# Kernel tuning notes

Measured on AMD Instinct MI355X. Metric: run time of the kernel, lower is better.

The kernel has to match this reference:

```python
import jax, jax.numpy as jnp
import numpy as np

N_NODES = 100000

def gcn_conv(x, W, b, src, dst):
    # PyG GCNConv: h = x @ W; add self-loops; symmetric norm D^-1/2 A D^-1/2; scatter-add; + bias
    n = x.shape[0]
    h = x @ W  # transform first (out_dim small) -> cheap messages
    loop = jnp.arange(n, dtype=src.dtype)
    s = jnp.concatenate([src, loop])
    d = jnp.concatenate([dst, loop])
    deg = jax.ops.segment_sum(jnp.ones_like(d, dtype=h.dtype), d, num_segments=n)
    dinv = jnp.where(deg > 0, jax.lax.rsqrt(deg), 0.0)
    norm = dinv[s] * dinv[d]  # [E+N]
    msg = h[s] * norm[:, None]  # gather + scale
    out = jax.ops.segment_sum(msg, d, num_segments=n)  # scatter-add to targets
    return out + b

def setup_inputs() -> dict:
    key = jax.random.key(0)
    k1, k2, k3, k4 = jax.random.split(key, 4)
    x = jax.random.normal(k1, (N_NODES, 128), dtype=jnp.float32)
    edge_index = jax.random.randint(k2, (2, 3200000), 0, N_NODES, dtype=jnp.int64)
    W1 = jax.random.normal(k3, (128, 16), dtype=jnp.float32) * 0.1
    b1 = jnp.zeros((16,), dtype=jnp.float32)
    W2 = jax.random.normal(k4, (16, 7), dtype=jnp.float32) * 0.1
    b2 = jnp.zeros((7,), dtype=jnp.float32)
    return {"x": x, "edge_index": edge_index, "W1": W1, "b1": b1, "W2": W2, "b2": b2}

def reference(x, edge_index, W1, b1, W2, b2):
    src, dst = edge_index[0], edge_index[1]
    h = gcn_conv(x, W1, b1, src, dst)
    h = jax.nn.relu(h)
    # F.dropout(training=self.training) is identity in eval mode
    h = gcn_conv(h, W2, b2, src, dst)
    return jax.nn.log_softmax(h, axis=1)
```

## Files before the change

kernel.cpp:

```cpp
#include <hip/hip_runtime.h>
#include <hip/hip_bf16.h>
#include <hip/hip_fp16.h>
#include <math.h>


#define FIN 128
#define FMID 16
#define FOUT 7

#define LBITS 7
#define NPB   128
#define SBITS 17
#define SMASK 0x1FFFF
#define NB_MAX 800
#define CAP   5120
#define EPT   12
#define BINT  1024
#define TILE  (EPT * BINT)

#define G1N   128
#define AS1   17
#define AS2   9

__global__ void zero_kernel(int* __restrict__ p, int m) {
    int i = blockIdx.x * 256 + threadIdx.x;
    if (i < m) p[i] = 0;
}

__device__ inline void addh8(float* a, float4 v) {
    const __half2* h = (const __half2*)&v;
#pragma unroll
    for (int k = 0; k < 4; ++k) {
        float2 f = __half22float2(h[k]);
        a[2 * k]     += f.x;
        a[2 * k + 1] += f.y;
    }
}

__global__ __launch_bounds__(BINT) void bin_kernel(const int* __restrict__ src,
                                                   const int* __restrict__ dst,
                                                   int* __restrict__ pairs,
                                                   int* __restrict__ gcnt,
                                                   int e, int nb) {
    __shared__ int sorted[TILE];
    __shared__ int cnt[NB_MAX], excl[NB_MAX], lofs[NB_MAX], gbase[NB_MAX];
    __shared__ int wsum[16];
    int tid = threadIdx.x;
    for (int j = tid; j < nb; j += BINT) cnt[j] = 0;
    __syncthreads();

    int base = blockIdx.x * TILE;
    int w[EPT], bk[EPT];
#pragma unroll
    for (int k = 0; k < EPT; ++k) {
        int idx = base + k * BINT + tid;
        if (idx < e) {
            int d = dst[idx], s = src[idx];
            w[k]  = ((d & (NPB - 1)) << SBITS) | s;
            bk[k] = d >> LBITS;
            atomicAdd(&cnt[bk[k]], 1);
        } else bk[k] = -1;
    }
    __syncthreads();

    if (tid < nb && cnt[tid] > 0) gbase[tid] = atomicAdd(&gcnt[tid], cnt[tid]);

    {
        int v = (tid < nb) ? cnt[tid] : 0;
        int lane = tid & 63, wid = tid >> 6;
        int incl = v;
#pragma unroll
        for (int d = 1; d < 64; d <<= 1) {
            int t = __shfl_up(incl, d);
            if (lane >= d) incl += t;
        }
        if (lane == 63) wsum[wid] = incl;
        __syncthreads();
        if (tid < 16) {
            int wv = wsum[tid];
            int wincl = wv;
#pragma unroll
            for (int d = 1; d < 16; d <<= 1) {
                int t = __shfl_up(wincl, d);
                if (tid >= d) wincl += t;
            }
            wsum[tid] = wincl - wv;
        }
        __syncthreads();
        if (tid < nb) {
            int ex = wsum[wid] + incl - v;
            excl[tid] = ex;
            lofs[tid] = ex;
        }
    }
    __syncthreads();

#pragma unroll
    for (int k = 0; k < EPT; ++k) {
        if (bk[k] >= 0) {
            int pos = atomicAdd(&lofs[bk[k]], 1);
            sorted[pos] = w[k];
        }
    }
    __syncthreads();

    int g16 = tid >> 4, l16 = tid & 15;
    for (int j = g16; j < nb; j += 64) {
        int c = cnt[j];
        if (!c) continue;
        int st = excl[j], gb = gbase[j];
        size_t go = (size_t)j * CAP;
        for (int l = l16; l < c; l += 16)
            if (gb + l < CAP) pairs[go + gb + l] = sorted[st + l];
    }
}

__global__ __launch_bounds__(512) void sort_kernel(int* __restrict__ pairs,
                                                   const int* __restrict__ gcnt,
                                                   int* __restrict__ rs_g,
                                                   float* __restrict__ dinv, int n) {
    __shared__ int slist[CAP];
    __shared__ int cnt2[NPB * 2], lofs2[NPB * 2], rowstart[NPB];
    __shared__ int wtot_s;
    int tid = threadIdx.x, b = blockIdx.x;
    int cc = tid & 1;
    if (tid < NPB * 2) cnt2[tid] = 0;
    __syncthreads();

    int c = min(gcnt[b], CAP);
    size_t go = (size_t)b * CAP;

    for (int i = tid; i < c; i += 512)
        atomicAdd(&cnt2[(pairs[go + i] >> SBITS) * 2 + cc], 1);
    __syncthreads();

    int v = 0, incl = 0;
    if (tid < NPB) {
        v = cnt2[tid * 2] + cnt2[tid * 2 + 1];
        incl = v;
        int lane = tid & 63;
#pragma unroll
        for (int d = 1; d < 64; d <<= 1) {
            int t = __shfl_up(incl, d);
            if (lane >= d) incl += t;
        }
        if (tid == 63) wtot_s = incl;
    }
    __syncthreads();
    if (tid < NPB) {
        int ex = incl - v + ((tid >= 64) ? wtot_s : 0);
        rowstart[tid] = ex;
        lofs2[tid * 2]     = ex;
        lofs2[tid * 2 + 1] = ex + cnt2[tid * 2];
    }
    __syncthreads();

    for (int i = tid; i < c; i += 512) {
        int w = pairs[go + i];
        int pos = atomicAdd(&lofs2[(w >> SBITS) * 2 + cc], 1);
        slist[pos] = w & SMASK;
    }
    __syncthreads();

    for (int i = tid; i < c; i += 512) pairs[go + i] = slist[i];
    if (tid < NPB) {
        rs_g[b * NPB + tid] = rowstart[tid];
        int node = b * NPB + tid;
        if (node < n) dinv[node] = rsqrtf((float)v + 1.0f);
    }
}

__global__ __launch_bounds__(256) void gemm1_kernel(const float* __restrict__ x,
                                                    const float* __restrict__ W,
                                                    const float* __restrict__ dinv,
                                                    __half* __restrict__ h1h, int n,
                                                    int sentinel) {
    __shared__ float WsT[16 * 132];
    int tid = threadIdx.x;
    int n0 = blockIdx.x * G1N;

    for (int i = tid; i < FIN * FMID; i += 256) {
        int k = i >> 4, f = i & 15;
        WsT[f * 132 + k] = W[i];
    }
    __syncthreads();

    int ngrp = tid >> 3;
    int fh = tid & 7;
    int r0 = n0 + ngrp, r1 = r0 + 32, r2 = r0 + 64, r3 = r0 + 96;
    int nc = n - 1;
    size_t c0 = (size_t)min(r0, nc) * 32;
    size_t c1 = (size_t)min(r1, nc) * 32;
    size_t c2 = (size_t)min(r2, nc) * 32;
    size_t c3 = (size_t)min(r3, nc) * 32;

    const float4* x4  = (const float4*)x;
    const float4* wa4 = (const float4*)(WsT + (2 * fh) * 132);
    const float4* wb4 = (const float4*)(WsT + (2 * fh + 1) * 132);

    float a0 = 0.f, a1 = 0.f, a2 = 0.f, a3 = 0.f;
    float b0 = 0.f, b1_ = 0.f, b2_ = 0.f, b3 = 0.f;

#pragma unroll 8
    for (int ck = 0; ck < 32; ++ck) {
        float4 x0 = x4[c0 + ck];
        float4 x1 = x4[c1 + ck];
        float4 x2 = x4[c2 + ck];
        float4 x3 = x4[c3 + ck];
        float4 wa = wa4[ck];
        float4 wb = wb4[ck];
        a0 += x0.x * wa.x + x0.y * wa.y + x0.z * wa.z + x0.w * wa.w;
        a1 += x1.x * wa.x + x1.y * wa.y + x1.z * wa.z + x1.w * wa.w;
        a2 += x2.x * wa.x + x2.y * wa.y + x2.z * wa.z + x2.w * wa.w;
        a3 += x3.x * wa.x + x3.y * wa.y + x3.z * wa.z + x3.w * wa.w;
        b0  += x0.x * wb.x + x0.y * wb.y + x0.z * wb.z + x0.w * wb.w;
        b1_ += x1.x * wb.x + x1.y * wb.y + x1.z * wb.z + x1.w * wb.w;
        b2_ += x2.x * wb.x + x2.y * wb.y + x2.z * wb.z + x2.w * wb.w;
        b3  += x3.x * wb.x + x3.y * wb.y + x3.z * wb.z + x3.w * wb.w;
    }

    float ra[4] = {a0, a1, a2, a3};
    float rb[4] = {b0, b1_, b2_, b3};
    int rr[4] = {r0, r1, r2, r3};
    __half2* h2 = (__half2*)h1h;
#pragma unroll
    for (int i = 0; i < 4; ++i) {
        int node = rr[i];
        if (node < n) {
            float dd = dinv ? dinv[node] : 1.0f;
            h2[(size_t)node * 8 + fh] = __floats2half2_rn(ra[i] * dd, rb[i] * dd);
        } else if (node == n && sentinel) {
            h2[(size_t)n * 8 + fh] = __floats2half2_rn(0.0f, 0.0f);
        }
    }
}

__global__ __launch_bounds__(512) void scatter1_kernel(const int* __restrict__ pairs,
                                                       const int* __restrict__ gcnt,
                                                       const int* __restrict__ rs_g,
                                                       const float* __restrict__ dinv,
                                                       const __half* __restrict__ h1h,
                                                       const float* __restrict__ b1,
                                                       const float* __restrict__ W2,
                                                       __half* __restrict__ h3h, int n) {
    __shared__ int   slist[CAP + 8];
    __shared__ int   rowstart_s[NPB + 1];
    __shared__ float acc2[NPB * AS1];
    __shared__ float W2s[FMID * FOUT];
    __shared__ float b1s[FMID];
    int tid = threadIdx.x, b = blockIdx.x;
    int c = min(gcnt[b], CAP);
    size_t go = (size_t)b * CAP;

    if (tid < FMID * FOUT) W2s[tid] = W2[tid];
    if (tid < FMID) b1s[tid] = b1[tid];
    if (tid < NPB) rowstart_s[tid] = rs_g[b * NPB + tid];
    if (tid == 0) rowstart_s[NPB] = c;
    for (int i = tid; i < c; i += 512) slist[i] = pairs[go + i];
    __syncthreads();

    {
        int nd = tid >> 2, l = tid & 3;
        int eo = l >> 1, half = l & 1;
        int pbeg = rowstart_s[nd];
        int pend = rowstart_s[nd + 1];
        const float4* h4 = (const float4*)h1h;
        float acc[8];
#pragma unroll
        for (int k = 0; k < 8; ++k) acc[k] = 0.0f;
        for (int p = pbeg + eo; p < pend; p += 8) {
            int i0 = slist[p];
            int i1 = (p + 2 < pend) ? slist[p + 2] : n;
            int i2 = (p + 4 < pend) ? slist[p + 4] : n;
            int i3 = (p + 6 < pend) ? slist[p + 6] : n;
            float4 v0 = h4[(size_t)i0 * 2 + half];
            float4 v1 = h4[(size_t)i1 * 2 + half];
            float4 v2 = h4[(size_t)i2 * 2 + half];
            float4 v3 = h4[(size_t)i3 * 2 + half];
            addh8(acc, v0);
            addh8(acc, v1);
            addh8(acc, v2);
            addh8(acc, v3);
        }
#pragma unroll
        for (int k = 0; k < 8; ++k) acc[k] += __shfl_xor(acc[k], 2);
        if (eo == 0) {
            float* ap = acc2 + nd * AS1 + half * 8;
#pragma unroll
            for (int k = 0; k < 8; ++k) ap[k] = acc[k];
        }
    }
    __syncthreads();

    int node = b * NPB + tid;
    if (tid < NPB && node < n) {
        float dd = dinv[node];
        float4 sr0 = ((const float4*)h1h)[(size_t)node * 2 + 0];
        float4 sr1 = ((const float4*)h1h)[(size_t)node * 2 + 1];
        float fself[FMID];
        {
            const __half2* ha = (const __half2*)&sr0;
            const __half2* hb = (const __half2*)&sr1;
#pragma unroll
            for (int k = 0; k < 4; ++k) {
                float2 fa = __half22float2(ha[k]);
                float2 fb = __half22float2(hb[k]);
                fself[2 * k]     = fa.x;
                fself[2 * k + 1] = fa.y;
                fself[8 + 2 * k]     = fb.x;
                fself[8 + 2 * k + 1] = fb.y;
            }
        }
        float vbuf[FMID];
#pragma unroll
        for (int k = 0; k < FMID; ++k) {
            float t = dd * (acc2[tid * AS1 + k] + fself[k]) + b1s[k];
            vbuf[k] = t > 0.0f ? t : 0.0f;
        }
        float sj[8];
#pragma unroll
        for (int j = 0; j < FOUT; ++j) {
            float s = 0.0f;
#pragma unroll
            for (int k = 0; k < FMID; ++k) s += vbuf[k] * W2s[k * FOUT + j];
            sj[j] = s * dd;
        }
        float4 st;
        __half2* sp = (__half2*)&st;
        sp[0] = __floats2half2_rn(sj[0], sj[1]);
        sp[1] = __floats2half2_rn(sj[2], sj[3]);
        sp[2] = __floats2half2_rn(sj[4], sj[5]);
        sp[3] = __floats2half2_rn(sj[6], 0.0f);
        ((float4*)h3h)[node] = st;
    } else if (tid < NPB && node == n) {
        ((float4*)h3h)[n] = make_float4(0.f, 0.f, 0.f, 0.f);
    }
}

__global__ __launch_bounds__(512) void scatter2_kernel(const int* __restrict__ pairs,
                                                       const int* __restrict__ gcnt,
                                                       const int* __restrict__ rs_g,
                                                       const float* __restrict__ dinv,
                                                       const __half* __restrict__ h3h,
                                                       const float* __restrict__ b2,
                                                       float* __restrict__ out, int n) {
    __shared__ int   slist[CAP + 8];
    __shared__ int   rowstart_s[NPB + 1];
    __shared__ float acc2[NPB * AS2];
    __shared__ float b2s[8];
    int tid = threadIdx.x, b = blockIdx.x;
    int c = min(gcnt[b], CAP);
    size_t go = (size_t)b * CAP;

    if (tid < FOUT) b2s[tid] = b2[tid];
    if (tid < NPB) rowstart_s[tid] = rs_g[b * NPB + tid];
    if (tid == 0) rowstart_s[NPB] = c;
    for (int i = tid; i < c; i += 512) slist[i] = pairs[go + i];
    __syncthreads();

    {
        int nd = tid >> 2, l = tid & 3;
        int pbeg = rowstart_s[nd];
        int pend = rowstart_s[nd + 1];
        const float4* h4 = (const float4*)h3h;
        float acc[8];
#pragma unroll
        for (int k = 0; k < 8; ++k) acc[k] = 0.0f;
        for (int p = pbeg + l; p < pend; p += 8) {
            int i0 = slist[p];
            int i1 = (p + 4 < pend) ? slist[p + 4] : n;
            float4 v0 = h4[i0];
            float4 v1 = h4[i1];
            addh8(acc, v0);
            addh8(acc, v1);
        }
#pragma unroll
        for (int k = 0; k < 8; ++k) {
            acc[k] += __shfl_xor(acc[k], 1);
            acc[k] += __shfl_xor(acc[k], 2);
        }
        if (l == 0) {
            float* ap = acc2 + nd * AS2;
#pragma unroll
            for (int k = 0; k < 8; ++k) ap[k] = acc[k];
        }
    }
    __syncthreads();

    int node = b * NPB + tid;
    if (tid < NPB && node < n) {
        float dd = dinv[node];
        float4 sv = ((const float4*)h3h)[node];
        float hself[8];
        {
            const __half2* h = (const __half2*)&sv;
#pragma unroll
            for (int k = 0; k < 4; ++k) {
                float2 f2v = __half22float2(h[k]);
                hself[2 * k] = f2v.x;
                hself[2 * k + 1] = f2v.y;
            }
        }
        float t[FOUT], m = -INFINITY;
#pragma unroll
        for (int j = 0; j < FOUT; ++j) {
            t[j] = dd * (acc2[tid * AS2 + j] + hself[j]) + b2s[j];
            m = fmaxf(m, t[j]);
        }
        float sum = 0.0f;
#pragma unroll
        for (int j = 0; j < FOUT; ++j) sum += expf(t[j] - m);
        float lse = logf(sum);
#pragma unroll
        for (int j = 0; j < FOUT; ++j) out[(size_t)node * FOUT + j] = t[j] - m - lse;
    }
}

__global__ void fb_gemm1_kernel(const float* __restrict__ x, const float* __restrict__ W,
                                float* __restrict__ h1, int n) {
    int i = blockIdx.x * blockDim.x + threadIdx.x;
    if (i >= n * FMID) return;
    int node = i >> 4, f = i & 15;
    float s = 0.0f;
    for (int k = 0; k < FIN; ++k) s += x[(size_t)node * FIN + k] * W[k * FMID + f];
    h1[i] = s;
}
__global__ void fb_deg_kernel(const int* __restrict__ dst, float* __restrict__ deg, int e) {
    int i = blockIdx.x * blockDim.x + threadIdx.x;
    if (i < e) atomicAdd(&deg[dst[i]], 1.0f);
}
__global__ void fb_dinv_kernel(float* __restrict__ deg, int n) {
    int i = blockIdx.x * blockDim.x + threadIdx.x;
    if (i < n) deg[i] = rsqrtf(deg[i] + 1.0f);
}
__global__ void fb_scatter1_kernel(const int* __restrict__ src, const int* __restrict__ dst,
                                   const float* __restrict__ dinv, const float* __restrict__ h1,
                                   float* __restrict__ out1, int e) {
    int i = blockIdx.x * blockDim.x + threadIdx.x;
    if (i >= e) return;
    int s = src[i], d = dst[i];
    float norm = dinv[s] * dinv[d];
    const float4* hs = (const float4*)(h1 + (size_t)s * FMID);
    float* o = out1 + (size_t)d * FMID;
#pragma unroll
    for (int q = 0; q < 4; ++q) {
        float4 vv = hs[q];
        atomicAdd(o + q * 4 + 0, vv.x * norm);
        atomicAdd(o + q * 4 + 1, vv.y * norm);
        atomicAdd(o + q * 4 + 2, vv.z * norm);
        atomicAdd(o + q * 4 + 3, vv.w * norm);
    }
}
__global__ void fb_layer2_kernel(const float* __restrict__ agg, const float* __restrict__ h1,
                                 const float* __restrict__ dinv, const float* __restrict__ b1,
                                 const float* __restrict__ W2, float* __restrict__ h3, int n) {
    int i = blockIdx.x * blockDim.x + threadIdx.x;
    if (i >= n) return;
    float dii = dinv[i] * dinv[i];
    float v[FMID];
#pragma unroll
    for (int k = 0; k < FMID; ++k) {
        float t = agg[(size_t)i * FMID + k] + h1[(size_t)i * FMID + k] * dii + b1[k];
        v[k] = t > 0.0f ? t : 0.0f;
    }
#pragma unroll
    for (int j = 0; j < FOUT; ++j) {
        float s = 0.0f;
#pragma unroll
        for (int k = 0; k < FMID; ++k) s += v[k] * W2[k * FOUT + j];
        h3[(size_t)i * FOUT + j] = s;
    }
}
__global__ void fb_scatter2_kernel(const int* __restrict__ src, const int* __restrict__ dst,
                                   const float* __restrict__ dinv, const float* __restrict__ h3,
                                   float* __restrict__ out2, int e) {
    int i = blockIdx.x * blockDim.x + threadIdx.x;
    if (i >= e) return;
    int s = src[i], d = dst[i];
    float norm = dinv[s] * dinv[d];
    const float* hs = h3 + (size_t)s * FOUT;
    float* o = out2 + (size_t)d * FOUT;
#pragma unroll
    for (int j = 0; j < FOUT; ++j) atomicAdd(o + j, hs[j] * norm);
}
__global__ void fb_finalize_kernel(const float* __restrict__ agg2, const float* __restrict__ h3,
                                   const float* __restrict__ dinv, const float* __restrict__ b2,
                                   float* __restrict__ out, int n) {
    int i = blockIdx.x * blockDim.x + threadIdx.x;
    if (i >= n) return;
    float dii = dinv[i] * dinv[i];
    float t[FOUT], m = -INFINITY;
#pragma unroll
    for (int j = 0; j < FOUT; ++j) {
        t[j] = agg2[(size_t)i * FOUT + j] + h3[(size_t)i * FOUT + j] * dii + b2[j];
        m = fmaxf(m, t[j]);
    }
    float sum = 0.0f;
#pragma unroll
    for (int j = 0; j < FOUT; ++j) sum += expf(t[j] - m);
    float lse = logf(sum);
#pragma unroll
    for (int j = 0; j < FOUT; ++j) out[(size_t)i * FOUT + j] = t[j] - m - lse;
}

extern "C" void kernel_launch(void* const* d_in, const int* in_sizes, int n_in,
                              void* d_out, int out_size, void* d_ws, size_t ws_size,
                              hipStream_t stream) {
    const float* x  = (const float*)d_in[0];
    const int*   ei = (const int*)d_in[1];
    const float* W1 = (const float*)d_in[2];
    const float* b1 = (const float*)d_in[3];
    const float* W2 = (const float*)d_in[4];
    const float* b2 = (const float*)d_in[5];

    const int n = in_sizes[0] / FIN;
    const int e = in_sizes[1] / 2;
    const int* src = ei;
    const int* dst = ei + e;

    const int nb  = (n + NPB - 1) / NPB;
    const int nb2 = (n + 1 + NPB - 1) / NPB;

    size_t need = ((size_t)NB_MAX + (size_t)nb * CAP + (size_t)n +
                   (size_t)nb2 * NPB + (size_t)8 * (n + 1) + (size_t)4 * (n + 1)) * 4;

    if (nb2 <= NB_MAX && n + 1 < (1 << SBITS) && ws_size >= need) {
        int*    gcnt  = (int*)d_ws;
        int*    pairs = gcnt + NB_MAX;
        float*  dinv  = (float*)(pairs + (size_t)nb * CAP);
        int*    rs_g  = (int*)(dinv + n);
        __half* h1h   = (__half*)(rs_g + (size_t)nb2 * NPB);
        __half* h3h   = h1h + (size_t)16 * (n + 1);

        zero_kernel<<<(NB_MAX + 255) / 256, 256, 0, stream>>>(gcnt, NB_MAX);

        int gridBin = (e + TILE - 1) / TILE;
        bin_kernel<<<gridBin, BINT, 0, stream>>>(src, dst, pairs, gcnt, e, nb);
        sort_kernel<<<nb, 512, 0, stream>>>(pairs, gcnt, rs_g, dinv, n);
        gemm1_kernel<<<nb2, 256, 0, stream>>>(x, W1, dinv, h1h, n, 1);
        scatter1_kernel<<<nb2, 512, 0, stream>>>(pairs, gcnt, rs_g, dinv, h1h, b1, W2, h3h, n);
        scatter2_kernel<<<nb, 512, 0, stream>>>(pairs, gcnt, rs_g, dinv, h3h, b2, (float*)d_out, n);
    } else {
        float* ws   = (float*)d_ws;
        float* deg  = ws;
        float* out1 = ws + (size_t)n;
        float* out2 = ws + (size_t)17 * n;
        float* h1   = ws + (size_t)24 * n;
        float* h3   = ws + (size_t)40 * n;

        hipMemsetAsync(ws, 0, (size_t)24 * n * sizeof(float), stream);

        const int B = 256;
        const int gridE = (e + B - 1) / B;
        const int gridN = (n + B - 1) / B;
        fb_deg_kernel<<<gridE, B, 0, stream>>>(dst, deg, e);
        fb_dinv_kernel<<<gridN, B, 0, stream>>>(deg, n);
        fb_gemm1_kernel<<<(n * FMID + B - 1) / B, B, 0, stream>>>(x, W1, h1, n);
        fb_scatter1_kernel<<<gridE, B, 0, stream>>>(src, dst, deg, h1, out1, e);
        fb_layer2_kernel<<<gridN, B, 0, stream>>>(out1, h1, deg, b1, W2, h3, n);
        fb_scatter2_kernel<<<gridE, B, 0, stream>>>(src, dst, deg, h3, out2, e);
        fb_finalize_kernel<<<gridN, B, 0, stream>>>(out2, h3, deg, b2, (float*)d_out, n);
    }
}
```

Measured before the change: 104.5 us.

## Fuse GCN pipeline into one cooperative persistent kernel with grid syncs

Replaces the six separate launches (zero, bin, sort, gemm1, scatter1, scatter2) with a single cooperative mega-kernel of 768 persistent blocks that separates the phases with grid-wide syncs. The aim is to remove kernel launch gaps and tail effects between phases. The binning phase now uses a smaller per-block tile with 512 threads. It also adds host-side occupancy and attribute queries on every call, and grid.sync has its own cost. It falls back to the old path if the cooperative launch is not possible.

New measurement: 104.7 us. About the same (+0.3%).

```diff
diff --git a/kernel.cpp b/kernel.cpp
--- a/kernel.cpp
+++ b/kernel.cpp
@@ -1,7 +1,10 @@
 #include <hip/hip_runtime.h>
 #include <hip/hip_bf16.h>
 #include <hip/hip_fp16.h>
+#include <hip/hip_cooperative_groups.h>
 #include <math.h>
+
+namespace cg = cooperative_groups;
 
 
 #define FIN 128
@@ -14,20 +17,20 @@
 #define SMASK 0x1FFFF
 #define NB_MAX 800
 #define CAP   5120
+#define AS1   17
+#define AS2   9
+
+#define MGRID 768
+#define MBLK  512
+#define BIN_TILE 5120
+#define SMEM_BYTES ((BIN_TILE + 4 * NB_MAX + 16) * 4)
+
 #define EPT   12
 #define BINT  1024
 #define TILE  (EPT * BINT)
-
 #define G1N   128
-#define AS1   17
-#define AS2   9
-
-__global__ void zero_kernel(int* __restrict__ p, int m) {
-    int i = blockIdx.x * 256 + threadIdx.x;
-    if (i < m) p[i] = 0;
-}
-
-__device__ inline void addh8(float* a, float4 v) {
+
+__device__ __forceinline__ void addh8(float* a, float4 v) {
     const __half2* h = (const __half2*)&v;
 #pragma unroll
     for (int k = 0; k < 4; ++k) {
@@ -35,6 +38,380 @@
         a[2 * k]     += f.x;
         a[2 * k + 1] += f.y;
     }
+}
+
+__device__ __forceinline__ int waveScanIncl(int v) {
+    int lane = threadIdx.x & 63;
+    int incl = v;
+#pragma unroll
+    for (int d = 1; d < 64; d <<= 1) {
+        int t = __shfl_up(incl, d);
+        if (lane >= d) incl += t;
+    }
+    return incl;
+}
+
+__device__ int scanEx512(int v, int* wsum, int* totalSlot) {
+    int tid = threadIdx.x;
+    int lane = tid & 63, wid = tid >> 6;
+    int incl = waveScanIncl(v);
+    if (lane == 63) wsum[wid] = incl;
+    __syncthreads();
+    if (tid == 0) {
+        int a = 0;
+#pragma unroll
+        for (int w = 0; w < 8; ++w) { int t = wsum[w]; wsum[w] = a; a += t; }
+        *totalSlot = a;
+    }
+    __syncthreads();
+    return wsum[wid] + incl - v;
+}
+
+__global__ __launch_bounds__(MBLK, 4) void mega_kernel(
+        const int* __restrict__ src, const int* __restrict__ dst,
+        const float* __restrict__ x, const float* __restrict__ W1,
+        const float* __restrict__ b1, const float* __restrict__ W2,
+        const float* __restrict__ b2,
+        int* __restrict__ pairs, int* __restrict__ gcnt,
+        int* __restrict__ rs_g, float* __restrict__ dinv,
+        __half* __restrict__ h1h, __half* __restrict__ h3h,
+        float* __restrict__ out, int n, int e, int nb) {
+    extern __shared__ int smem[];
+    cg::grid_group grid = cg::this_grid();
+    int tid = threadIdx.x;
+
+    if (blockIdx.x == 0)
+        for (int i = tid; i < NB_MAX; i += MBLK) gcnt[i] = 0;
+    grid.sync();
+
+    {
+        int* sorted = smem;
+        int* cnt    = sorted + BIN_TILE;
+        int* excl   = cnt + NB_MAX;
+        int* lofs   = excl + NB_MAX;
+        int* gbase  = lofs + NB_MAX;
+        int* wsum   = gbase + NB_MAX;
+        int* tots   = wsum + 8;
+
+        int tileM = (e + MGRID - 1) / MGRID;
+        int base  = blockIdx.x * tileM;
+        int mycnt = e - base;
+        if (mycnt > tileM) mycnt = tileM;
+        if (mycnt < 0) mycnt = 0;
+
+        for (int j = tid; j < nb; j += MBLK) cnt[j] = 0;
+        __syncthreads();
+        for (int i = tid; i < mycnt; i += MBLK)
+            atomicAdd(&cnt[dst[base + i] >> LBITS], 1);
+        __syncthreads();
+        for (int j = tid; j < nb; j += MBLK) {
+            int cj = cnt[j];
+            if (cj > 0) gbase[j] = atomicAdd(&gcnt[j], cj);
+        }
+        int v0 = (tid < nb) ? cnt[tid] : 0;
+        int ex0 = scanEx512(v0, wsum, &tots[0]);
+        if (tid < nb) { excl[tid] = ex0; lofs[tid] = ex0; }
+        __syncthreads();
+        int j2 = tid + MBLK;
+        int v1 = (j2 < nb) ? cnt[j2] : 0;
+        int ex1 = scanEx512(v1, wsum, &tots[1]);
+        int t0 = tots[0];
+        if (j2 < nb) { excl[j2] = t0 + ex1; lofs[j2] = t0 + ex1; }
+        __syncthreads();
+        for (int i = tid; i < mycnt; i += MBLK) {
+            int d = dst[base + i], s = src[base + i];
+            int w = ((d & (NPB - 1)) << SBITS) | s;
+            int pos = atomicAdd(&lofs[d >> LBITS], 1);
+            sorted[pos] = w;
+        }
+        __syncthreads();
+        int g8 = tid >> 3, l8 = tid & 7;
+        for (int j = g8; j < nb; j += 64) {
+            int cj = cnt[j];
+            if (!cj) continue;
+            int st = excl[j], gb = gbase[j];
+            size_t go = (size_t)j * CAP;
+            for (int l = l8; l < cj; l += 8)
+                if (gb + l < CAP) pairs[go + gb + l] = sorted[st + l];
+        }
+    }
+    grid.sync();
+
+    {
+        int* slist    = smem;
+        int* cnt2     = slist + CAP;
+        int* lofs2    = cnt2 + 256;
+        int* rowstart = lofs2 + 256;
+        int* wtot     = rowstart + NPB;
+        for (int b = blockIdx.x; b < nb; b += MGRID) {
+            __syncthreads();
+            if (tid < NPB * 2) cnt2[tid] = 0;
+            __syncthreads();
+            int c = min(gcnt[b], CAP);
+            size_t go = (size_t)b * CAP;
+            int cc = tid & 1;
+            for (int i = tid; i < c; i += MBLK)
+                atomicAdd(&cnt2[(pairs[go + i] >> SBITS) * 2 + cc], 1);
+            __syncthreads();
+            int v = 0, incl = 0;
+            if (tid < NPB) {
+                v = cnt2[tid * 2] + cnt2[tid * 2 + 1];
+                incl = waveScanIncl(v);
+                if (tid == 63) *wtot = incl;
+            }
+            __syncthreads();
+            if (tid < NPB) {
+                int ex = incl - v + ((tid >= 64) ? *wtot : 0);
+                rowstart[tid] = ex;
+                lofs2[tid * 2]     = ex;
+                lofs2[tid * 2 + 1] = ex + cnt2[tid * 2];
+            }
+            __syncthreads();
+            for (int i = tid; i < c; i += MBLK) {
+                int w = pairs[go + i];
+                int pos = atomicAdd(&lofs2[(w >> SBITS) * 2 + cc], 1);
+                slist[pos] = w & SMASK;
+            }
+            __syncthreads();
+            for (int i = tid; i < c; i += MBLK) pairs[go + i] = slist[i];
+            if (tid < NPB) {
+                rs_g[b * NPB + tid] = rowstart[tid];
+                int node = b * NPB + tid;
+                if (node < n) dinv[node] = rsqrtf((float)v + 1.0f);
+            }
+        }
+    }
+    grid.sync();
+
+    {
+        float* WsT = (float*)smem;
+        for (int i = tid; i < FIN * FMID; i += MBLK) {
+            int k = i >> 4, f = i & 15;
+            WsT[f * 132 + k] = W1[i];
+        }
+        __syncthreads();
+        int nvb = (n + 1 + 255) / 256;
+        int ngrp = tid >> 3;
+        int fh = tid & 7;
+        int nc = n - 1;
+        const float4* x4  = (const float4*)x;
+        const float4* wa4 = (const float4*)(WsT + (2 * fh) * 132);
+        const float4* wb4 = (const float4*)(WsT + (2 * fh + 1) * 132);
+        __half2* h2 = (__half2*)h1h;
+        for (int vb = blockIdx.x; vb < nvb; vb += MGRID) {
+            int n0 = vb * 256;
+            int r0 = n0 + ngrp, r1 = r0 + 64, r2 = r0 + 128, r3 = r0 + 192;
+            size_t c0 = (size_t)min(r0, nc) * 32;
+            size_t c1 = (size_t)min(r1, nc) * 32;
+            size_t c2 = (size_t)min(r2, nc) * 32;
+            size_t c3 = (size_t)min(r3, nc) * 32;
+            float a0 = 0.f, a1 = 0.f, a2 = 0.f, a3 = 0.f;
+            float b0 = 0.f, b1_ = 0.f, b2_ = 0.f, b3_ = 0.f;
+#pragma unroll 8
+            for (int ck = 0; ck < 32; ++ck) {
+                float4 x0 = x4[c0 + ck];
+                float4 x1 = x4[c1 + ck];
+                float4 x2 = x4[c2 + ck];
+                float4 x3 = x4[c3 + ck];
+                float4 wa = wa4[ck];
+                float4 wb = wb4[ck];
+                a0 += x0.x * wa.x + x0.y * wa.y + x0.z * wa.z + x0.w * wa.w;
+                a1 += x1.x * wa.x + x1.y * wa.y + x1.z * wa.z + x1.w * wa.w;
+                a2 += x2.x * wa.x + x2.y * wa.y + x2.z * wa.z + x2.w * wa.w;
+                a3 += x3.x * wa.x + x3.y * wa.y + x3.z * wa.z + x3.w * wa.w;
+                b0  += x0.x * wb.x + x0.y * wb.y + x0.z * wb.z + x0.w * wb.w;
+                b1_ += x1.x * wb.x + x1.y * wb.y + x1.z * wb.z + x1.w * wb.w;
+                b2_ += x2.x * wb.x + x2.y * wb.y + x2.z * wb.z + x2.w * wb.w;
+                b3_ += x3.x * wb.x + x3.y * wb.y + x3.z * wb.z + x3.w * wb.w;
+            }
+            float ra[4] = {a0, a1, a2, a3};
+            float rb[4] = {b0, b1_, b2_, b3_};
+            int rr[4] = {r0, r1, r2, r3};
+#pragma unroll
+            for (int i2 = 0; i2 < 4; ++i2) {
+                int node = rr[i2];
+                if (node < n) {
+                    float dd = dinv[node];
+                    h2[(size_t)node * 8 + fh] = __floats2half2_rn(ra[i2] * dd, rb[i2] * dd);
+                } else if (node == n) {
+                    h2[(size_t)n * 8 + fh] = __floats2half2_rn(0.0f, 0.0f);
+                }
+            }
+        }
+    }
+    grid.sync();
+
+    {
+        int*   slist    = smem;
+        int*   rowstart = slist + CAP + 8;
+        float* acc2     = (float*)(rowstart + NPB + 1);
+        float* W2s      = acc2 + NPB * AS1;
+        float* b1s      = W2s + FMID * FOUT;
+        if (tid < FMID * FOUT) W2s[tid] = W2[tid];
+        if (tid < FMID) b1s[tid] = b1[tid];
+        for (int b = blockIdx.x; b < nb; b += MGRID) {
+            __syncthreads();
+            int c = min(gcnt[b], CAP);
+            size_t go = (size_t)b * CAP;
+            if (tid < NPB) rowstart[tid] = rs_g[b * NPB + tid];
+            if (tid == 0) rowstart[NPB] = c;
+            for (int i = tid; i < c; i += MBLK) slist[i] = pairs[go + i];
+            __syncthreads();
+            {
+                int nd = tid >> 2, l = tid & 3;
+                int eo = l >> 1, half = l & 1;
+                int pbeg = rowstart[nd];
+                int pend = rowstart[nd + 1];
+                const float4* h4 = (const float4*)h1h;
+                float acc[8];
+#pragma unroll
+                for (int k = 0; k < 8; ++k) acc[k] = 0.0f;
+                for (int p = pbeg + eo; p < pend; p += 8) {
+                    int i0 = slist[p];
+                    int i1 = (p + 2 < pend) ? slist[p + 2] : n;
+                    int i2 = (p + 4 < pend) ? slist[p + 4] : n;
+                    int i3 = (p + 6 < pend) ? slist[p + 6] : n;
+                    float4 v0 = h4[(size_t)i0 * 2 + half];
+                    float4 v1 = h4[(size_t)i1 * 2 + half];
+                    float4 v2 = h4[(size_t)i2 * 2 + half];
+                    float4 v3 = h4[(size_t)i3 * 2 + half];
+                    addh8(acc, v0);
+                    addh8(acc, v1);
+                    addh8(acc, v2);
+                    addh8(acc, v3);
+                }
+#pragma unroll
+                for (int k = 0; k < 8; ++k) acc[k] += __shfl_xor(acc[k], 2);
+                if (eo == 0) {
+                    float* ap = acc2 + nd * AS1 + half * 8;
+#pragma unroll
+                    for (int k = 0; k < 8; ++k) ap[k] = acc[k];
+                }
+            }
+            __syncthreads();
+            int node = b * NPB + tid;
+            if (tid < NPB && node < n) {
+                float dd = dinv[node];
+                float4 sr0 = ((const float4*)h1h)[(size_t)node * 2 + 0];
+                float4 sr1 = ((const float4*)h1h)[(size_t)node * 2 + 1];
+                float fself[FMID];
+                {
+                    const __half2* ha = (const __half2*)&sr0;
+                    const __half2* hb = (const __half2*)&sr1;
+#pragma unroll
+                    for (int k = 0; k < 4; ++k) {
+                        float2 fa = __half22float2(ha[k]);
+                        float2 fb = __half22float2(hb[k]);
+                        fself[2 * k]     = fa.x;
+                        fself[2 * k + 1] = fa.y;
+                        fself[8 + 2 * k]     = fb.x;
+                        fself[8 + 2 * k + 1] = fb.y;
+                    }
+                }
+                float vbuf[FMID];
+#pragma unroll
+                for (int k = 0; k < FMID; ++k) {
+                    float t = dd * (acc2[tid * AS1 + k] + fself[k]) + b1s[k];
+                    vbuf[k] = t > 0.0f ? t : 0.0f;
+                }
+                float sj[8];
+#pragma unroll
+                for (int j = 0; j < FOUT; ++j) {
+                    float s = 0.0f;
+#pragma unroll
+                    for (int k = 0; k < FMID; ++k) s += vbuf[k] * W2s[k * FOUT + j];
+                    sj[j] = s * dd;
+                }
+                float4 st;
+                __half2* sp = (__half2*)&st;
+                sp[0] = __floats2half2_rn(sj[0], sj[1]);
+                sp[1] = __floats2half2_rn(sj[2], sj[3]);
+                sp[2] = __floats2half2_rn(sj[4], sj[5]);
+                sp[3] = __floats2half2_rn(sj[6], 0.0f);
+                ((float4*)h3h)[node] = st;
+            } else if (tid < NPB && node == n) {
+                ((float4*)h3h)[n] = make_float4(0.f, 0.f, 0.f, 0.f);
+            }
+        }
+    }
+    grid.sync();
+
+    {
+        int*   slist    = smem;
+        int*   rowstart = slist + CAP + 8;
+        float* acc2     = (float*)(rowstart + NPB + 1);
+        float* b2s      = acc2 + NPB * AS2;
+        if (tid < FOUT) b2s[tid] = b2[tid];
+        for (int b = blockIdx.x; b < nb; b += MGRID) {
+            __syncthreads();
+            int c = min(gcnt[b], CAP);
+            size_t go = (size_t)b * CAP;
+            if (tid < NPB) rowstart[tid] = rs_g[b * NPB + tid];
+            if (tid == 0) rowstart[NPB] = c;
+            for (int i = tid; i < c; i += MBLK) slist[i] = pairs[go + i];
+            __syncthreads();
+            {
+                int nd = tid >> 2, l = tid & 3;
+                int pbeg = rowstart[nd];
+                int pend = rowstart[nd + 1];
+                const float4* h4 = (const float4*)h3h;
+                float acc[8];
+#pragma unroll
+                for (int k = 0; k < 8; ++k) acc[k] = 0.0f;
+                for (int p = pbeg + l; p < pend; p += 8) {
+                    int i0 = slist[p];
+                    int i1 = (p + 4 < pend) ? slist[p + 4] : n;
+                    float4 v0 = h4[i0];
+                    float4 v1 = h4[i1];
+                    addh8(acc, v0);
+                    addh8(acc, v1);
+                }
+#pragma unroll
+                for (int k = 0; k < 8; ++k) {
+                    acc[k] += __shfl_xor(acc[k], 1);
+                    acc[k] += __shfl_xor(acc[k], 2);
+                }
+                if (l == 0) {
+                    float* ap = acc2 + nd * AS2;
+#pragma unroll
+                    for (int k = 0; k < 8; ++k) ap[k] = acc[k];
+                }
+            }
+            __syncthreads();
+            int node = b * NPB + tid;
+            if (tid < NPB && node < n) {
+                float dd = dinv[node];
+                float4 sv = ((const float4*)h3h)[node];
+                float hself[8];
+                {
+                    const __half2* h = (const __half2*)&sv;
+#pragma unroll
+                    for (int k = 0; k < 4; ++k) {
+                        float2 f2v = __half22float2(h[k]);
+                        hself[2 * k] = f2v.x;
+                        hself[2 * k + 1] = f2v.y;
+                    }
+                }
+                float t[FOUT], m = -INFINITY;
+#pragma unroll
+                for (int j = 0; j < FOUT; ++j) {
+                    t[j] = dd * (acc2[tid * AS2 + j] + hself[j]) + b2s[j];
+                    m = fmaxf(m, t[j]);
+                }
+                float sum = 0.0f;
+#pragma unroll
+                for (int j = 0; j < FOUT; ++j) sum += expf(t[j] - m);
+                float lse = logf(sum);
+#pragma unroll
+                for (int j = 0; j < FOUT; ++j) out[(size_t)node * FOUT + j] = t[j] - m - lse;
+            }
+        }
+    }
+}
+
+__global__ void zero_kernel(int* __restrict__ p, int m) {
+    int i = blockIdx.x * 256 + threadIdx.x;
+    if (i < m) p[i] = 0;
 }
 
 __global__ __launch_bounds__(BINT) void bin_kernel(const int* __restrict__ src,
@@ -532,8 +909,42 @@
         __half* h1h   = (__half*)(rs_g + (size_t)nb2 * NPB);
         __half* h3h   = h1h + (size_t)16 * (n + 1);
 
+        int mega_ok = 0;
+        if (nb2 == nb && (long)e <= (long)MGRID * BIN_TILE) {
+            int dev = 0;
+            if (hipGetDevice(&dev) == hipSuccess) {
+                int coop = 0;
+                hipDeviceGetAttribute(&coop, hipDeviceAttributeCooperativeLaunch, dev);
+                if (coop) {
+                    int mab = 0;
+                    if (hipOccupancyMaxActiveBlocksPerMultiprocessor(
+                            &mab, mega_kernel, MBLK, (size_t)SMEM_BYTES) == hipSuccess) {
+                        int ncu = 0;
+                        hipDeviceGetAttribute(&ncu, hipDeviceAttributeMultiprocessorCount, dev);
+                        if ((long)mab * ncu >= MGRID) mega_ok = 1;
+                    }
+                }
+            }
+        }
+
+        if (mega_ok) {
+            const int* k_src = src; const int* k_dst = dst;
+            const float* k_x = x; const float* k_W1 = W1; const float* k_b1 = b1;
+            const float* k_W2 = W2; const float* k_b2 = b2;
+            int* k_pairs = pairs; int* k_gcnt = gcnt; int* k_rsg = rs_g;
+            float* k_dinv = dinv; __half* k_h1 = h1h; __half* k_h3 = h3h;
+            float* k_out = (float*)d_out;
+            int k_n = n, k_e = e, k_nb = nb;
+            void* args[] = {&k_src, &k_dst, &k_x, &k_W1, &k_b1, &k_W2, &k_b2,
+                            &k_pairs, &k_gcnt, &k_rsg, &k_dinv, &k_h1, &k_h3,
+                            &k_out, &k_n, &k_e, &k_nb};
+            hipError_t lerr = hipLaunchCooperativeKernel(
+                (const void*)mega_kernel, dim3(MGRID), dim3(MBLK),
+                args, (unsigned)SMEM_BYTES, stream);
+            if (lerr == hipSuccess) return;
+        }
+
         zero_kernel<<<(NB_MAX + 255) / 256, 256, 0, stream>>>(gcnt, NB_MAX);
-
         int gridBin = (e + TILE - 1) / TILE;
         bin_kernel<<<gridBin, BINT, 0, stream>>>(src, dst, pairs, gcnt, e, nb);
         sort_kernel<<<nb, 512, 0, stream>>>(pairs, gcnt, rs_g, dinv, n);
```
